# Kernel optimization log

Hardware: AMD Instinct MI355X
Metric: run time of the kernel (lower is better)

The kernel has to match this reference:

```python
import jax, jax.numpy as jnp
import numpy as np

NUM_GRAPHS = 64
NODE_SZ = 200
FEAT = 200
HID = 256          # hidden_size; each signed branch outputs HID//2
HALF = HID // 2
N_NODES = NUM_GRAPHS * NODE_SZ
N_EDGES = 409600
NUM_LAYERS = 3


def _lin_init(key, out_f, in_f):
    kw, kb = jax.random.split(key)
    s = 1.0 / np.sqrt(in_f)
    W = jax.random.uniform(kw, (out_f, in_f), minval=-s, maxval=s, dtype=jnp.float32)
    b = jax.random.uniform(kb, (out_f,), minval=-s, maxval=s, dtype=jnp.float32)
    return W, b


def setup_inputs() -> dict:
    key = jax.random.key(0)
    ks = jax.random.split(key, 16)
    x = jax.random.normal(ks[0], (N_NODES, FEAT), dtype=jnp.float32)
    edge_index = jax.random.randint(ks[1], (2, N_EDGES), 0, N_NODES, dtype=jnp.int64)
    edge_weight = jax.random.normal(ks[2], (N_EDGES,), dtype=jnp.float32)
    batch = jnp.repeat(jnp.arange(NUM_GRAPHS, dtype=jnp.int64), NODE_SZ)

    # signed conv layer params: layer0 in=FEAT, layers 1..: in=HID; each lin maps 2*in -> HALF
    Wp0, bp0 = _lin_init(ks[3], HALF, 2 * FEAT)
    Wn0, bn0 = _lin_init(ks[4], HALF, 2 * FEAT)
    Wp1, bp1 = _lin_init(ks[5], HALF, 2 * HID)
    Wn1, bn1 = _lin_init(ks[6], HALF, 2 * HID)
    Wp2, bp2 = _lin_init(ks[7], HALF, 2 * HID)
    Wn2, bn2 = _lin_init(ks[8], HALF, 2 * HID)
    Wr, br = _lin_init(ks[9], HID, NODE_SZ * HID)   # readout_lin
    Wl, bl = _lin_init(ks[10], 1, HID)              # final lin
    return dict(x=x, edge_index=edge_index, edge_weight=edge_weight, batch=batch,
                Wp0=Wp0, bp0=bp0, Wn0=Wn0, bn0=bn0,
                Wp1=Wp1, bp1=bp1, Wn1=Wn1, bn1=bn1,
                Wp2=Wp2, bp2=bp2, Wn2=Wn2, bn2=bn2,
                Wr=Wr, br=br, Wl=Wl, bl=bl)


def _signed_conv(x, src, dst, w, Wp, bp, Wn, bn):
    # edge-weighted signed mean aggregation, split by weight sign
    xs = x[src]                                   # [E, D] gather
    pw = jnp.where(w > 0, w, 0.0)
    nw = jnp.where(w < 0, -w, 0.0)
    agg_p = jax.ops.segment_sum(pw[:, None] * xs, dst, num_segments=N_NODES)
    agg_n = jax.ops.segment_sum(nw[:, None] * xs, dst, num_segments=N_NODES)
    deg_p = jax.ops.segment_sum((w > 0).astype(x.dtype), dst, num_segments=N_NODES)
    deg_n = jax.ops.segment_sum((w < 0).astype(x.dtype), dst, num_segments=N_NODES)
    agg_p = agg_p / jnp.maximum(deg_p, 1.0)[:, None]
    agg_n = agg_n / jnp.maximum(deg_n, 1.0)[:, None]
    hp = jnp.concatenate([agg_p, x], -1) @ Wp.T + bp
    hn = jnp.concatenate([agg_n, x], -1) @ Wn.T + bn
    return jnp.concatenate([hp, hn], -1)          # [N, HID]


def reference(x, edge_index, edge_weight, batch,
              Wp0, bp0, Wn0, bn0, Wp1, bp1, Wn1, bn1, Wp2, bp2, Wn2, bn2,
              Wr, br, Wl, bl):
    src, dst = edge_index[0], edge_index[1]
    convs = [(Wp0, bp0, Wn0, bn0), (Wp1, bp1, Wn1, bn1), (Wp2, bp2, Wn2, bn2)]
    h = x
    for i, (Wp, bp, Wn, bn) in enumerate(convs):
        h = _signed_conv(h, src, dst, edge_weight, Wp, bp, Wn, bn)
        if i < NUM_LAYERS - 1:
            h = jax.nn.leaky_relu(h, negative_slope=0.01)
    # per-graph readout: batch is contiguous with NODE_SZ nodes per graph,
    # so the boolean-mask+view loop is exactly a reshape.
    g = h.reshape(NUM_GRAPHS, NODE_SZ * HID)
    g = g @ Wr.T + br                             # [G, HID]
    # dropout(p=0.5) is identity in eval mode
    return g @ Wl.T + bl                          # [G, 1]
```

## Files before the change

kernel.cpp:

```cpp
#include <hip/hip_runtime.h>

#define NUM_GRAPHS 64
#define NODE_SZ    200
#define FEAT       200
#define HID        256
#define HALF       128
#define N_NODES    (NUM_GRAPHS * NODE_SZ)
#define KREAD      (NODE_SZ * HID)
#define HBLK       128

typedef unsigned short ushort_t;
typedef unsigned int uint_t;
typedef __attribute__((ext_vector_type(8))) short bf16x8;
typedef __attribute__((ext_vector_type(4))) float f32x4;

#define GAS(p) ((const __attribute__((address_space(1))) void*)(p))
#define LAS(p) ((__attribute__((address_space(3))) void*)(p))

__device__ __forceinline__ float bf2f(ushort_t u) {
    union { unsigned int i; float f; } v; v.i = ((unsigned int)u) << 16; return v.f;
}
__device__ __forceinline__ ushort_t f2bf(float f) {
    union { float f; unsigned int i; } v; v.f = f;
    unsigned int x = v.i;
    unsigned int r = (x + 0x7fffu + ((x >> 16) & 1u)) >> 16;
    return (ushort_t)r;
}

__global__ __launch_bounds__(1024) void bhist_kernel(const int* __restrict__ ei,
                                                     const float* __restrict__ ew,
                                                     uint_t* __restrict__ bh, int E) {
    __shared__ uint_t h[N_NODES];
    for (int i = threadIdx.x; i < N_NODES; i += 1024) h[i] = 0;
    __syncthreads();
    int b = blockIdx.x;
    int epb = (E + HBLK - 1) / HBLK;
    int e0 = b * epb, e1 = min(e0 + epb, E);
    for (int e = e0 + threadIdx.x; e < e1; e += 1024) {
        int dst = ei[E + e];
        float w = ew[e];
        if (w > 0.0f)      atomicAdd(&h[dst], 1u);
        else if (w < 0.0f) atomicAdd(&h[dst], 0x10000u);
    }
    __syncthreads();
    uint_t* out = bh + (size_t)b * N_NODES;
    for (int i = threadIdx.x * 4; i < N_NODES; i += 4096)
        *(uint4*)&out[i] = *(const uint4*)&h[i];
}

__global__ void colpref_kernel(uint_t* __restrict__ bh, int* __restrict__ counts,
                               int* __restrict__ cnt_p) {
    int n = blockIdx.x * 256 + threadIdx.x;
    if (n >= N_NODES) return;
    uint_t seq = 0;
#pragma unroll 1
    for (int b = 0; b < HBLK; b += 8) {
        uint_t v[8];
#pragma unroll
        for (int j = 0; j < 8; ++j) v[j] = bh[(size_t)(b + j) * N_NODES + n];
#pragma unroll
        for (int j = 0; j < 8; ++j) {
            bh[(size_t)(b + j) * N_NODES + n] = seq;
            seq += v[j];
        }
    }
    counts[n] = (int)((seq & 0xffffu) + (seq >> 16));
    cnt_p[n]  = (int)(seq & 0xffffu);
}

__global__ __launch_bounds__(1024) void scan_kernel(const int* __restrict__ counts,
                                                    const int* __restrict__ cnt_p,
                                                    uint2* __restrict__ obnd, int n) {
    const int PER = 13;
    int t = threadIdx.x;
    int start = t * PER;
    int local[PER];
    int sum = 0;
#pragma unroll
    for (int i = 0; i < PER; ++i) {
        int idx = start + i;
        int v = (idx < n) ? counts[idx] : 0;
        local[i] = sum;
        sum += v;
    }
    int lane = t & 63, wid = t >> 6;
    int inc = sum;
#pragma unroll
    for (int d = 1; d < 64; d <<= 1) {
        int up = __shfl_up(inc, d);
        if (lane >= d) inc += up;
    }
    __shared__ int wsum[16], woff[16];
    if (lane == 63) wsum[wid] = inc;
    __syncthreads();
    if (t < 16) {
        int acc = 0;
        for (int j = 0; j < 16; ++j) if (j < t) acc += wsum[j];
        woff[t] = acc;
    }
    __syncthreads();
    int base = woff[wid] + (inc - sum);
#pragma unroll
    for (int i = 0; i < PER; ++i) {
        int idx = start + i;
        if (idx < n) {
            uint_t off = (uint_t)(base + local[i]);
            obnd[idx] = make_uint2(off, off + (uint_t)cnt_p[idx]);
        }
    }
    if (t == 1023) {
        uint_t tot = (uint_t)(base + sum);
        obnd[n] = make_uint2(tot, tot);
    }
}

__global__ __launch_bounds__(1024) void scat_prep_kernel(
        const int* __restrict__ ei, const float* __restrict__ ew,
        const uint_t* __restrict__ bh, const uint2* __restrict__ obnd,
        uint2* __restrict__ es, int E,
        const float* __restrict__ W0p, const float* __restrict__ W0n,
        const float* __restrict__ W1p, const float* __restrict__ W1n,
        const float* __restrict__ W2p, const float* __restrict__ W2n,
        const float* __restrict__ x,
        ushort_t* __restrict__ wall, ushort_t* __restrict__ xb) {
    __shared__ uint_t cur[N_NODES];
    int bx = blockIdx.x;
    if (bx < HBLK) {
        const uint_t* pref = bh + (size_t)bx * N_NODES;
        for (int i = threadIdx.x * 4; i < N_NODES; i += 4096)
            *(uint4*)&cur[i] = *(const uint4*)&pref[i];
        __syncthreads();
        int epb = (E + HBLK - 1) / HBLK;
        int e0 = bx * epb, e1 = min(e0 + epb, E);
        for (int e = e0 + threadIdx.x; e < e1; e += 1024) {
            int src = ei[e];
            int dst = ei[E + e];
            float w = ew[e];
            if (w > 0.0f) {
                uint_t old = atomicAdd(&cur[dst], 1u);
                uint_t pos = obnd[dst].x + (old & 0xffffu);
                es[pos] = make_uint2((uint_t)src, __float_as_uint(w));
            } else if (w < 0.0f) {
                uint_t old = atomicAdd(&cur[dst], 0x10000u);
                uint_t pos = obnd[dst].y + (old >> 16);
                es[pos] = make_uint2((uint_t)src, __float_as_uint(-w));
            }
        }
    } else if (bx < 512) {
        int idx = (bx - 128) * 1024 + threadIdx.x;
        int layer = idx >> 17;
        int within = idx & 131071;
        int rr = within >> 8;
        int col = within & 255;
        const float* Wp = (layer == 0) ? W0p : (layer == 1) ? W1p : W2p;
        const float* Wn = (layer == 0) ? W0n : (layer == 1) ? W1n : W2n;
        int Ks = (layer == 0) ? 200 : 256;
        int q = rr >> 7;
        const float* Wsrc = (q & 1) ? Wn : Wp;
        int row = rr & 127;
        int scol = col + ((q >> 1) ? Ks : 0);
        float v = (col < Ks) ? Wsrc[(size_t)row * (2 * Ks) + scol] : 0.0f;
        wall[idx] = f2bf(v);
    } else {
        int idx = (bx - 512) * 1024 + threadIdx.x;
        int n = idx >> 6;
        int c0 = (idx & 63) * 4;
        ushort4 o = {0, 0, 0, 0};
        if (c0 < 200) {
            float4 v = *(const float4*)&x[(size_t)n * 200 + c0];
            o.x = f2bf(v.x); o.y = f2bf(v.y); o.z = f2bf(v.z); o.w = f2bf(v.w);
        }
        *(ushort4*)&xb[(size_t)n * 256 + c0] = o;
    }
}

template <int KSTEPS>
__global__ __launch_bounds__(256) void gemm_mfma(
        const ushort_t* __restrict__ A,
        const ushort_t* __restrict__ B,
        ushort_t* __restrict__ Y) {
    __shared__ __align__(16) ushort_t As[2][32 * 32];
    __shared__ __align__(16) ushort_t Bs[2][128 * 32];
    int mBase = blockIdx.x * 32;
    int nBase = blockIdx.y * 128;
    int tid  = threadIdx.x;
    int lane = tid & 63;
    int wv   = tid >> 6;
    int r    = lane & 15;
    int quad = lane >> 4;

    int rowA = tid >> 2, colA = (tid & 3) * 8;
    const ushort_t* gA  = A + (size_t)(mBase + (rowA & 31)) * 256 + colA;
    const ushort_t* gB0 = B + (size_t)(nBase + rowA) * 256 + colA;
    const ushort_t* gB1 = B + (size_t)(nBase + rowA + 64) * 256 + colA;

    f32x4 acc00 = {0.f,0.f,0.f,0.f}, acc01 = {0.f,0.f,0.f,0.f};
    f32x4 acc10 = {0.f,0.f,0.f,0.f}, acc11 = {0.f,0.f,0.f,0.f};

    if (tid < 128)
        __builtin_amdgcn_global_load_lds(GAS(gA), LAS(&As[0][wv * 512]), 16, 0, 0);
    __builtin_amdgcn_global_load_lds(GAS(gB0), LAS(&Bs[0][wv * 512]), 16, 0, 0);
    __builtin_amdgcn_global_load_lds(GAS(gB1), LAS(&Bs[0][2048 + wv * 512]), 16, 0, 0);

    for (int kt = 0; kt < KSTEPS; ++kt) {
        int cur = kt & 1;
        __syncthreads();
        if (kt + 1 < KSTEPS) {
            int kB = (kt + 1) * 32;
            if (tid < 128)
                __builtin_amdgcn_global_load_lds(GAS(gA + kB), LAS(&As[cur ^ 1][wv * 512]), 16, 0, 0);
            __builtin_amdgcn_global_load_lds(GAS(gB0 + kB), LAS(&Bs[cur ^ 1][wv * 512]), 16, 0, 0);
            __builtin_amdgcn_global_load_lds(GAS(gB1 + kB), LAS(&Bs[cur ^ 1][2048 + wv * 512]), 16, 0, 0);
        }
        bf16x8 a0 = *(const bf16x8*)&As[cur][r * 32 + quad * 8];
        bf16x8 a1 = *(const bf16x8*)&As[cur][(16 + r) * 32 + quad * 8];
        bf16x8 b0 = *(const bf16x8*)&Bs[cur][(wv * 32 + r) * 32 + quad * 8];
        bf16x8 b1 = *(const bf16x8*)&Bs[cur][(wv * 32 + 16 + r) * 32 + quad * 8];
        acc00 = __builtin_amdgcn_mfma_f32_16x16x32_bf16(a0, b0, acc00, 0, 0, 0);
        acc01 = __builtin_amdgcn_mfma_f32_16x16x32_bf16(a0, b1, acc01, 0, 0, 0);
        acc10 = __builtin_amdgcn_mfma_f32_16x16x32_bf16(a1, b0, acc10, 0, 0, 0);
        acc11 = __builtin_amdgcn_mfma_f32_16x16x32_bf16(a1, b1, acc11, 0, 0, 0);
    }
#pragma unroll
    for (int jn = 0; jn < 2; ++jn) {
        int cl = nBase + wv * 32 + jn * 16 + r;
        f32x4 am0 = jn ? acc01 : acc00;
        f32x4 am1 = jn ? acc11 : acc10;
#pragma unroll
        for (int reg = 0; reg < 4; ++reg) {
            int m0 = mBase + quad * 4 + reg;
            Y[(size_t)m0 * 512 + cl]        = f2bf(am0[reg]);
            Y[(size_t)(m0 + 16) * 512 + cl] = f2bf(am1[reg]);
        }
    }
}

template <bool LEAKY>
__global__ __launch_bounds__(256) void aggcomb_kernel(
        const ushort_t* __restrict__ Y,
        const uint2* __restrict__ obnd,
        const uint2* __restrict__ es,
        const float* __restrict__ bp, const float* __restrict__ bn,
        ushort_t* __restrict__ out) {
    int lane = threadIdx.x & 63;
    int wv   = threadIdx.x >> 6;
    int n = blockIdx.x * 4 + wv;
    int c0 = lane * 2;
    uint2 ob = obnd[n];
    uint_t off = ob.x, mid = ob.y, end = obnd[n + 1].x;

    float accp[2] = {0.f, 0.f};
    float accn[2] = {0.f, 0.f};

#pragma unroll 1
    for (int phase = 0; phase < 2; ++phase) {
        uint_t lo = phase ? mid : off;
        uint_t hi = phase ? end : mid;
        float* acc = phase ? accn : accp;
        const ushort_t* Yb = Y + (phase ? 128 : 0) + c0;
#pragma unroll 1
        for (uint_t base = lo; base < hi; base += 64) {
            int cnt = (int)min(64u, hi - base);
            uint2 rec = es[base + (uint_t)min(lane, cnt - 1)];
            int i = 0;
#pragma unroll 1
            for (; i + 8 <= cnt; i += 8) {
                int s[8]; float w[8]; uint_t u[8];
#pragma unroll
                for (int j = 0; j < 8; ++j) {
                    s[j] = __shfl((int)rec.x, i + j);
                    w[j] = __uint_as_float((uint_t)__shfl((int)rec.y, i + j));
                }
#pragma unroll
                for (int j = 0; j < 8; ++j) u[j] = *(const uint_t*)&Yb[(size_t)s[j] * 512];
#pragma unroll
                for (int j = 0; j < 8; ++j) {
                    acc[0] = fmaf(w[j], bf2f((ushort_t)(u[j] & 0xffffu)), acc[0]);
                    acc[1] = fmaf(w[j], bf2f((ushort_t)(u[j] >> 16)), acc[1]);
                }
            }
#pragma unroll 1
            for (; i < cnt; ++i) {
                int s = __shfl((int)rec.x, i);
                float w = __uint_as_float((uint_t)__shfl((int)rec.y, i));
                uint_t u = *(const uint_t*)&Yb[(size_t)s * 512];
                acc[0] = fmaf(w, bf2f((ushort_t)(u & 0xffffu)), acc[0]);
                acc[1] = fmaf(w, bf2f((ushort_t)(u >> 16)), acc[1]);
            }
        }
    }

    float dp = fmaxf((float)(mid - off), 1.0f);
    float dn = fmaxf((float)(end - mid), 1.0f);
    float rp = 1.0f / dp, rn = 1.0f / dn;
    uint_t zp = *(const uint_t*)&Y[(size_t)n * 512 + 256 + c0];
    uint_t zn = *(const uint_t*)&Y[(size_t)n * 512 + 384 + c0];
    float vp0 = fmaf(accp[0], rp, bf2f((ushort_t)(zp & 0xffffu)) + bp[c0]);
    float vp1 = fmaf(accp[1], rp, bf2f((ushort_t)(zp >> 16))     + bp[c0 + 1]);
    float vn0 = fmaf(accn[0], rn, bf2f((ushort_t)(zn & 0xffffu)) + bn[c0]);
    float vn1 = fmaf(accn[1], rn, bf2f((ushort_t)(zn >> 16))     + bn[c0 + 1]);
    if (LEAKY) {
        vp0 = (vp0 > 0.0f) ? vp0 : 0.01f * vp0;
        vp1 = (vp1 > 0.0f) ? vp1 : 0.01f * vp1;
        vn0 = (vn0 > 0.0f) ? vn0 : 0.01f * vn0;
        vn1 = (vn1 > 0.0f) ? vn1 : 0.01f * vn1;
    }
    uint_t op = (uint_t)f2bf(vp0) | ((uint_t)f2bf(vp1) << 16);
    uint_t on = (uint_t)f2bf(vn0) | ((uint_t)f2bf(vn1) << 16);
    *(uint_t*)&out[(size_t)n * 256 + c0]       = op;
    *(uint_t*)&out[(size_t)n * 256 + 128 + c0] = on;
}

__global__ __launch_bounds__(256) void readout_mfma(
        const ushort_t* __restrict__ h, const float* __restrict__ Wr,
        float* __restrict__ partial) {
    __shared__ __align__(16) ushort_t As[64 * 32];
    __shared__ __align__(16) ushort_t Bs[64 * 32];
    int nBase  = blockIdx.x * 64;
    int kStart = blockIdx.y * 800;
    int tid  = threadIdx.x;
    int lane = tid & 63;
    int wv   = tid >> 6;
    int r    = lane & 15;
    int quad = lane >> 4;

    f32x4 acc[4];
#pragma unroll
    for (int j = 0; j < 4; ++j) acc[j] = (f32x4){0.f, 0.f, 0.f, 0.f};

    for (int kt = 0; kt < 25; ++kt) {
        int kBase = kStart + kt * 32;
        int lin = tid * 8;
        int row = lin >> 5, col = lin & 31;
        *(uint4*)&As[lin] = *(const uint4*)&h[(size_t)row * KREAD + kBase + col];
        {
            const float* wp = &Wr[(size_t)(nBase + row) * KREAD + kBase + col];
            float4 f0 = *(const float4*)&wp[0];
            float4 f1 = *(const float4*)&wp[4];
            ushort4 b0, b1;
            b0.x = f2bf(f0.x); b0.y = f2bf(f0.y); b0.z = f2bf(f0.z); b0.w = f2bf(f0.w);
            b1.x = f2bf(f1.x); b1.y = f2bf(f1.y); b1.z = f2bf(f1.z); b1.w = f2bf(f1.w);
            *(ushort4*)&Bs[lin]     = b0;
            *(ushort4*)&Bs[lin + 4] = b1;
        }
        __syncthreads();
        bf16x8 a = *(const bf16x8*)&As[(wv * 16 + r) * 32 + quad * 8];
#pragma unroll
        for (int j = 0; j < 4; ++j) {
            bf16x8 b = *(const bf16x8*)&Bs[(j * 16 + r) * 32 + quad * 8];
            acc[j] = __builtin_amdgcn_mfma_f32_16x16x32_bf16(a, b, acc[j], 0, 0, 0);
        }
        __syncthreads();
    }
    float* out = partial + (size_t)blockIdx.y * (64 * HID);
#pragma unroll
    for (int j = 0; j < 4; ++j) {
        int c = nBase + j * 16 + r;
#pragma unroll
        for (int reg = 0; reg < 4; ++reg) {
            int g = wv * 16 + quad * 4 + reg;
            out[g * HID + c] = acc[j][reg];
        }
    }
}

__global__ void final_kernel(const float* __restrict__ partial, const float* __restrict__ br,
                             const float* __restrict__ Wl, const float* __restrict__ bl,
                             float* __restrict__ out) {
    int g = blockIdx.x;
    int c = threadIdx.x;
    float s = 0.0f;
#pragma unroll 4
    for (int k = 0; k < 64; ++k) s += partial[(size_t)k * (64 * HID) + g * HID + c];
    float v = (s + br[c]) * Wl[c];
#pragma unroll
    for (int d = 32; d > 0; d >>= 1) v += __shfl_down(v, d);
    __shared__ float sh[4];
    if ((c & 63) == 0) sh[c >> 6] = v;
    __syncthreads();
    if (c == 0) out[g] = sh[0] + sh[1] + sh[2] + sh[3] + bl[0];
}

extern "C" void kernel_launch(void* const* d_in, const int* in_sizes, int n_in,
                              void* d_out, int out_size, void* d_ws, size_t ws_size,
                              hipStream_t stream) {
    const float* x  = (const float*)d_in[0];
    const int*   ei = (const int*)d_in[1];
    const float* ew = (const float*)d_in[2];
    const float* Wp0 = (const float*)d_in[4];
    const float* bp0 = (const float*)d_in[5];
    const float* Wn0 = (const float*)d_in[6];
    const float* bn0 = (const float*)d_in[7];
    const float* Wp1 = (const float*)d_in[8];
    const float* bp1 = (const float*)d_in[9];
    const float* Wn1 = (const float*)d_in[10];
    const float* bn1 = (const float*)d_in[11];
    const float* Wp2 = (const float*)d_in[12];
    const float* bp2 = (const float*)d_in[13];
    const float* Wn2 = (const float*)d_in[14];
    const float* bn2 = (const float*)d_in[15];
    const float* Wr  = (const float*)d_in[16];
    const float* br  = (const float*)d_in[17];
    const float* Wl  = (const float*)d_in[18];
    const float* bl  = (const float*)d_in[19];
    const int E = in_sizes[1] / 2;

    char* ws = (char*)d_ws;
    float*    partial = (float*)(ws + 0);
    uint_t*   bh      = (uint_t*)(ws + 4194304);
    int*      counts  = (int*)(ws + 10747904);
    int*      cnt_p   = (int*)(ws + 10799104);
    uint2*    obnd    = (uint2*)(ws + 10850304);
    uint2*    es      = (uint2*)(ws + 10952768);
    ushort_t* Yall    = (ushort_t*)(ws + 14229568);
    ushort_t* hA      = (ushort_t*)(ws + 27336768);
    ushort_t* hB      = (ushort_t*)(ws + 33890368);
    ushort_t* wall    = (ushort_t*)(ws + 40443968);
    ushort_t* xb      = (ushort_t*)(ws + 41230400);

    hipLaunchKernelGGL(bhist_kernel, dim3(HBLK), dim3(1024), 0, stream, ei, ew, bh, E);
    hipLaunchKernelGGL(colpref_kernel, dim3((N_NODES + 255) / 256), dim3(256), 0, stream,
                       bh, counts, cnt_p);
    hipLaunchKernelGGL(scan_kernel, dim3(1), dim3(1024), 0, stream, counts, cnt_p, obnd, N_NODES);
    hipLaunchKernelGGL(scat_prep_kernel, dim3(1312), dim3(1024), 0, stream,
                       ei, ew, bh, obnd, es, E,
                       Wp0, Wn0, Wp1, Wn1, Wp2, Wn2, x, wall, xb);

    hipLaunchKernelGGL((gemm_mfma<7>), dim3(N_NODES / 32, 4), dim3(256), 0, stream,
                       xb, wall + 0 * 131072, Yall);
    hipLaunchKernelGGL((aggcomb_kernel<true>), dim3(N_NODES / 4), dim3(256), 0, stream,
                       Yall, obnd, es, bp0, bn0, hA);
    hipLaunchKernelGGL((gemm_mfma<8>), dim3(N_NODES / 32, 4), dim3(256), 0, stream,
                       hA, wall + 1 * 131072, Yall);
    hipLaunchKernelGGL((aggcomb_kernel<true>), dim3(N_NODES / 4), dim3(256), 0, stream,
                       Yall, obnd, es, bp1, bn1, hB);
    hipLaunchKernelGGL((gemm_mfma<8>), dim3(N_NODES / 32, 4), dim3(256), 0, stream,
                       hB, wall + 2 * 131072, Yall);
    hipLaunchKernelGGL((aggcomb_kernel<false>), dim3(N_NODES / 4), dim3(256), 0, stream,
                       Yall, obnd, es, bp2, bn2, hA);

    hipLaunchKernelGGL(readout_mfma, dim3(4, 64), dim3(256), 0, stream, hA, Wr, partial);
    hipLaunchKernelGGL(final_kernel, dim3(NUM_GRAPHS), dim3(256), 0, stream,
                       partial, br, Wl, bl, (float*)d_out);
}
```

Baseline: 296.8 us.

## Fuse whole pipeline into one persistent kernel with software grid barriers

Replaces the chain of about a dozen kernel launches with an init kernel plus one persistent mega-kernel of 256 blocks. Phases are separated by flag-based global barriers. The CSR build now uses global atomics for the histogram and a two-level block scan instead of per-block LDS histograms. The GEMM is retiled to 128x256 tiles over 200 tiles, and aggregation uses a grid-stride loop. This removes launch gaps and per-kernel tail effects. In exchange it risks barrier spin cost and global atomic contention, and it relies on all 256 blocks being co-resident, which a barrier with a timeout cap does not guarantee.

Result: slower. 1.176 ms (+296.3%).

```diff
diff --git a/kernel.cpp b/kernel.cpp
--- a/kernel.cpp
+++ b/kernel.cpp
@@ -7,7 +7,8 @@
 #define HALF       128
 #define N_NODES    (NUM_GRAPHS * NODE_SZ)
 #define KREAD      (NODE_SZ * HID)
-#define HBLK       128
+#define NBLK       256
+#define NTHR       512
 
 typedef unsigned short ushort_t;
 typedef unsigned int uint_t;
@@ -27,313 +28,190 @@
     return (ushort_t)r;
 }
 
-__global__ __launch_bounds__(1024) void bhist_kernel(const int* __restrict__ ei,
-                                                     const float* __restrict__ ew,
-                                                     uint_t* __restrict__ bh, int E) {
-    __shared__ uint_t h[N_NODES];
-    for (int i = threadIdx.x; i < N_NODES; i += 1024) h[i] = 0;
+__device__ __forceinline__ void gbar(uint_t* __restrict__ flags, int k) {
+    __threadfence();
     __syncthreads();
-    int b = blockIdx.x;
-    int epb = (E + HBLK - 1) / HBLK;
-    int e0 = b * epb, e1 = min(e0 + epb, E);
-    for (int e = e0 + threadIdx.x; e < e1; e += 1024) {
-        int dst = ei[E + e];
-        float w = ew[e];
-        if (w > 0.0f)      atomicAdd(&h[dst], 1u);
-        else if (w < 0.0f) atomicAdd(&h[dst], 0x10000u);
+    if (threadIdx.x == 0)
+        __hip_atomic_store(&flags[(k << 8) | blockIdx.x], 1u,
+                           __ATOMIC_RELAXED, __HIP_MEMORY_SCOPE_AGENT);
+    if (threadIdx.x < NBLK) {
+        int cap = 0;
+        while (__hip_atomic_load(&flags[(k << 8) | threadIdx.x],
+                                 __ATOMIC_RELAXED, __HIP_MEMORY_SCOPE_AGENT) == 0u) {
+            __builtin_amdgcn_s_sleep(2);
+            if (++cap > (1 << 18)) break;
+        }
     }
     __syncthreads();
-    uint_t* out = bh + (size_t)b * N_NODES;
-    for (int i = threadIdx.x * 4; i < N_NODES; i += 4096)
-        *(uint4*)&out[i] = *(const uint4*)&h[i];
-}
-
-__global__ void colpref_kernel(uint_t* __restrict__ bh, int* __restrict__ counts,
-                               int* __restrict__ cnt_p) {
-    int n = blockIdx.x * 256 + threadIdx.x;
-    if (n >= N_NODES) return;
-    uint_t seq = 0;
-#pragma unroll 1
-    for (int b = 0; b < HBLK; b += 8) {
-        uint_t v[8];
-#pragma unroll
-        for (int j = 0; j < 8; ++j) v[j] = bh[(size_t)(b + j) * N_NODES + n];
-#pragma unroll
-        for (int j = 0; j < 8; ++j) {
-            bh[(size_t)(b + j) * N_NODES + n] = seq;
-            seq += v[j];
-        }
-    }
-    counts[n] = (int)((seq & 0xffffu) + (seq >> 16));
-    cnt_p[n]  = (int)(seq & 0xffffu);
-}
-
-__global__ __launch_bounds__(1024) void scan_kernel(const int* __restrict__ counts,
-                                                    const int* __restrict__ cnt_p,
-                                                    uint2* __restrict__ obnd, int n) {
-    const int PER = 13;
-    int t = threadIdx.x;
-    int start = t * PER;
-    int local[PER];
-    int sum = 0;
-#pragma unroll
-    for (int i = 0; i < PER; ++i) {
-        int idx = start + i;
-        int v = (idx < n) ? counts[idx] : 0;
-        local[i] = sum;
-        sum += v;
-    }
-    int lane = t & 63, wid = t >> 6;
-    int inc = sum;
-#pragma unroll
-    for (int d = 1; d < 64; d <<= 1) {
-        int up = __shfl_up(inc, d);
-        if (lane >= d) inc += up;
-    }
-    __shared__ int wsum[16], woff[16];
-    if (lane == 63) wsum[wid] = inc;
-    __syncthreads();
-    if (t < 16) {
-        int acc = 0;
-        for (int j = 0; j < 16; ++j) if (j < t) acc += wsum[j];
-        woff[t] = acc;
-    }
-    __syncthreads();
-    int base = woff[wid] + (inc - sum);
-#pragma unroll
-    for (int i = 0; i < PER; ++i) {
-        int idx = start + i;
-        if (idx < n) {
-            uint_t off = (uint_t)(base + local[i]);
-            obnd[idx] = make_uint2(off, off + (uint_t)cnt_p[idx]);
-        }
-    }
-    if (t == 1023) {
-        uint_t tot = (uint_t)(base + sum);
-        obnd[n] = make_uint2(tot, tot);
-    }
-}
-
-__global__ __launch_bounds__(1024) void scat_prep_kernel(
-        const int* __restrict__ ei, const float* __restrict__ ew,
-        const uint_t* __restrict__ bh, const uint2* __restrict__ obnd,
-        uint2* __restrict__ es, int E,
-        const float* __restrict__ W0p, const float* __restrict__ W0n,
-        const float* __restrict__ W1p, const float* __restrict__ W1n,
-        const float* __restrict__ W2p, const float* __restrict__ W2n,
-        const float* __restrict__ x,
-        ushort_t* __restrict__ wall, ushort_t* __restrict__ xb) {
-    __shared__ uint_t cur[N_NODES];
-    int bx = blockIdx.x;
-    if (bx < HBLK) {
-        const uint_t* pref = bh + (size_t)bx * N_NODES;
-        for (int i = threadIdx.x * 4; i < N_NODES; i += 4096)
-            *(uint4*)&cur[i] = *(const uint4*)&pref[i];
-        __syncthreads();
-        int epb = (E + HBLK - 1) / HBLK;
-        int e0 = bx * epb, e1 = min(e0 + epb, E);
-        for (int e = e0 + threadIdx.x; e < e1; e += 1024) {
-            int src = ei[e];
-            int dst = ei[E + e];
-            float w = ew[e];
-            if (w > 0.0f) {
-                uint_t old = atomicAdd(&cur[dst], 1u);
-                uint_t pos = obnd[dst].x + (old & 0xffffu);
-                es[pos] = make_uint2((uint_t)src, __float_as_uint(w));
-            } else if (w < 0.0f) {
-                uint_t old = atomicAdd(&cur[dst], 0x10000u);
-                uint_t pos = obnd[dst].y + (old >> 16);
-                es[pos] = make_uint2((uint_t)src, __float_as_uint(-w));
-            }
-        }
-    } else if (bx < 512) {
-        int idx = (bx - 128) * 1024 + threadIdx.x;
-        int layer = idx >> 17;
-        int within = idx & 131071;
-        int rr = within >> 8;
-        int col = within & 255;
-        const float* Wp = (layer == 0) ? W0p : (layer == 1) ? W1p : W2p;
-        const float* Wn = (layer == 0) ? W0n : (layer == 1) ? W1n : W2n;
-        int Ks = (layer == 0) ? 200 : 256;
-        int q = rr >> 7;
-        const float* Wsrc = (q & 1) ? Wn : Wp;
-        int row = rr & 127;
-        int scol = col + ((q >> 1) ? Ks : 0);
-        float v = (col < Ks) ? Wsrc[(size_t)row * (2 * Ks) + scol] : 0.0f;
-        wall[idx] = f2bf(v);
-    } else {
-        int idx = (bx - 512) * 1024 + threadIdx.x;
-        int n = idx >> 6;
-        int c0 = (idx & 63) * 4;
-        ushort4 o = {0, 0, 0, 0};
-        if (c0 < 200) {
-            float4 v = *(const float4*)&x[(size_t)n * 200 + c0];
-            o.x = f2bf(v.x); o.y = f2bf(v.y); o.z = f2bf(v.z); o.w = f2bf(v.w);
-        }
-        *(ushort4*)&xb[(size_t)n * 256 + c0] = o;
-    }
-}
-
-template <int KSTEPS>
-__global__ __launch_bounds__(256) void gemm_mfma(
-        const ushort_t* __restrict__ A,
-        const ushort_t* __restrict__ B,
-        ushort_t* __restrict__ Y) {
-    __shared__ __align__(16) ushort_t As[2][32 * 32];
-    __shared__ __align__(16) ushort_t Bs[2][128 * 32];
-    int mBase = blockIdx.x * 32;
-    int nBase = blockIdx.y * 128;
+    __threadfence();
+}
+
+__device__ __forceinline__ void gemm_phase(const ushort_t* __restrict__ A,
+                                           const ushort_t* __restrict__ Bw,
+                                           ushort_t* __restrict__ Y,
+                                           ushort_t* smem) {
+    int t = blockIdx.x;
+    if (t >= 200) return;
+    int mBase = (t >> 1) * 128;
+    int nBase = (t & 1) * 256;
     int tid  = threadIdx.x;
     int lane = tid & 63;
     int wv   = tid >> 6;
     int r    = lane & 15;
     int quad = lane >> 4;
-
-    int rowA = tid >> 2, colA = (tid & 3) * 8;
-    const ushort_t* gA  = A + (size_t)(mBase + (rowA & 31)) * 256 + colA;
-    const ushort_t* gB0 = B + (size_t)(nBase + rowA) * 256 + colA;
-    const ushort_t* gB1 = B + (size_t)(nBase + rowA + 64) * 256 + colA;
-
-    f32x4 acc00 = {0.f,0.f,0.f,0.f}, acc01 = {0.f,0.f,0.f,0.f};
-    f32x4 acc10 = {0.f,0.f,0.f,0.f}, acc11 = {0.f,0.f,0.f,0.f};
-
-    if (tid < 128)
-        __builtin_amdgcn_global_load_lds(GAS(gA), LAS(&As[0][wv * 512]), 16, 0, 0);
-    __builtin_amdgcn_global_load_lds(GAS(gB0), LAS(&Bs[0][wv * 512]), 16, 0, 0);
-    __builtin_amdgcn_global_load_lds(GAS(gB1), LAS(&Bs[0][2048 + wv * 512]), 16, 0, 0);
-
-    for (int kt = 0; kt < KSTEPS; ++kt) {
-        int cur = kt & 1;
+    int wm   = wv >> 1;
+    int wn   = wv & 1;
+
+    int rowA = tid >> 2, colc = (tid & 3) * 8;
+    const ushort_t* gA  = A  + (size_t)(mBase + rowA) * 256 + colc;
+    const ushort_t* gB0 = Bw + (size_t)(nBase + rowA) * 256 + colc;
+    const ushort_t* gB1 = Bw + (size_t)(nBase + 128 + rowA) * 256 + colc;
+
+    f32x4 acc[2][8];
+#pragma unroll
+    for (int i = 0; i < 2; ++i)
+#pragma unroll
+        for (int j = 0; j < 8; ++j) acc[i][j] = (f32x4){0.f, 0.f, 0.f, 0.f};
+
+    auto STAGE = [&](int buf, int kb) {
+        ushort_t* Ad = smem + (buf << 12) + tid * 8;
+        ushort_t* Bd = smem + 8192 + (buf << 13) + tid * 8;
+        __builtin_amdgcn_global_load_lds(GAS(gA + kb), LAS(Ad), 16, 0, 0);
+        __builtin_amdgcn_global_load_lds(GAS(gB0 + kb), LAS(Bd), 16, 0, 0);
+        __builtin_amdgcn_global_load_lds(GAS(gB1 + kb), LAS(Bd + 4096), 16, 0, 0);
+    };
+
+    STAGE(0, 0);
+    for (int kt = 0; kt < 8; ++kt) {
+        int cb = kt & 1;
         __syncthreads();
-        if (kt + 1 < KSTEPS) {
-            int kB = (kt + 1) * 32;
-            if (tid < 128)
-                __builtin_amdgcn_global_load_lds(GAS(gA + kB), LAS(&As[cur ^ 1][wv * 512]), 16, 0, 0);
-            __builtin_amdgcn_global_load_lds(GAS(gB0 + kB), LAS(&Bs[cur ^ 1][wv * 512]), 16, 0, 0);
-            __builtin_amdgcn_global_load_lds(GAS(gB1 + kB), LAS(&Bs[cur ^ 1][2048 + wv * 512]), 16, 0, 0);
-        }
-        bf16x8 a0 = *(const bf16x8*)&As[cur][r * 32 + quad * 8];
-        bf16x8 a1 = *(const bf16x8*)&As[cur][(16 + r) * 32 + quad * 8];
-        bf16x8 b0 = *(const bf16x8*)&Bs[cur][(wv * 32 + r) * 32 + quad * 8];
-        bf16x8 b1 = *(const bf16x8*)&Bs[cur][(wv * 32 + 16 + r) * 32 + quad * 8];
-        acc00 = __builtin_amdgcn_mfma_f32_16x16x32_bf16(a0, b0, acc00, 0, 0, 0);
-        acc01 = __builtin_amdgcn_mfma_f32_16x16x32_bf16(a0, b1, acc01, 0, 0, 0);
-        acc10 = __builtin_amdgcn_mfma_f32_16x16x32_bf16(a1, b0, acc10, 0, 0, 0);
-        acc11 = __builtin_amdgcn_mfma_f32_16x16x32_bf16(a1, b1, acc11, 0, 0, 0);
-    }
-#pragma unroll
-    for (int jn = 0; jn < 2; ++jn) {
-        int cl = nBase + wv * 32 + jn * 16 + r;
-        f32x4 am0 = jn ? acc01 : acc00;
-        f32x4 am1 = jn ? acc11 : acc10;
-#pragma unroll
-        for (int reg = 0; reg < 4; ++reg) {
-            int m0 = mBase + quad * 4 + reg;
-            Y[(size_t)m0 * 512 + cl]        = f2bf(am0[reg]);
-            Y[(size_t)(m0 + 16) * 512 + cl] = f2bf(am1[reg]);
-        }
-    }
-}
-
-template <bool LEAKY>
-__global__ __launch_bounds__(256) void aggcomb_kernel(
-        const ushort_t* __restrict__ Y,
-        const uint2* __restrict__ obnd,
-        const uint2* __restrict__ es,
-        const float* __restrict__ bp, const float* __restrict__ bn,
-        ushort_t* __restrict__ out) {
+        if (kt < 7) STAGE(cb ^ 1, (kt + 1) * 32);
+        const ushort_t* Ac = smem + (cb << 12);
+        const ushort_t* Bc = smem + 8192 + (cb << 13);
+        bf16x8 af[2];
+#pragma unroll
+        for (int i = 0; i < 2; ++i)
+            af[i] = *(const bf16x8*)&Ac[(wm * 32 + i * 16 + r) * 32 + quad * 8];
+#pragma unroll
+        for (int j = 0; j < 8; ++j) {
+            bf16x8 bfr = *(const bf16x8*)&Bc[(wn * 128 + j * 16 + r) * 32 + quad * 8];
+            acc[0][j] = __builtin_amdgcn_mfma_f32_16x16x32_bf16(af[0], bfr, acc[0][j], 0, 0, 0);
+            acc[1][j] = __builtin_amdgcn_mfma_f32_16x16x32_bf16(af[1], bfr, acc[1][j], 0, 0, 0);
+        }
+    }
+#pragma unroll
+    for (int i = 0; i < 2; ++i)
+#pragma unroll
+        for (int j = 0; j < 8; ++j) {
+            int c = nBase + wn * 128 + j * 16 + r;
+#pragma unroll
+            for (int reg = 0; reg < 4; ++reg) {
+                int m = mBase + wm * 32 + i * 16 + quad * 4 + reg;
+                Y[(size_t)m * 512 + c] = f2bf(acc[i][j][reg]);
+            }
+        }
+}
+
+__device__ __forceinline__ void agg_phase(const ushort_t* __restrict__ Y,
+                                          const uint2* __restrict__ obnd,
+                                          const uint2* __restrict__ es,
+                                          const float* __restrict__ bp,
+                                          const float* __restrict__ bn,
+                                          ushort_t* __restrict__ outp, bool leaky) {
     int lane = threadIdx.x & 63;
-    int wv   = threadIdx.x >> 6;
-    int n = blockIdx.x * 4 + wv;
     int c0 = lane * 2;
-    uint2 ob = obnd[n];
-    uint_t off = ob.x, mid = ob.y, end = obnd[n + 1].x;
-
-    float accp[2] = {0.f, 0.f};
-    float accn[2] = {0.f, 0.f};
-
+    int nw = gridDim.x << 3;
+    for (int n = (blockIdx.x << 3) + (threadIdx.x >> 6); n < N_NODES; n += nw) {
+        uint2 ob = obnd[n];
+        uint_t off = ob.x, mid = ob.y, end = obnd[n + 1].x;
+        float accp[2] = {0.f, 0.f};
+        float accn[2] = {0.f, 0.f};
 #pragma unroll 1
-    for (int phase = 0; phase < 2; ++phase) {
-        uint_t lo = phase ? mid : off;
-        uint_t hi = phase ? end : mid;
-        float* acc = phase ? accn : accp;
-        const ushort_t* Yb = Y + (phase ? 128 : 0) + c0;
+        for (int phase = 0; phase < 2; ++phase) {
+            uint_t lo = phase ? mid : off;
+            uint_t hi = phase ? end : mid;
+            float* acc = phase ? accn : accp;
+            const ushort_t* Yb = Y + (phase ? 128 : 0) + c0;
 #pragma unroll 1
-        for (uint_t base = lo; base < hi; base += 64) {
-            int cnt = (int)min(64u, hi - base);
-            uint2 rec = es[base + (uint_t)min(lane, cnt - 1)];
-            int i = 0;
+            for (uint_t base = lo; base < hi; base += 64) {
+                int cnt = (int)min(64u, hi - base);
+                uint2 rec = es[base + (uint_t)min(lane, cnt - 1)];
+                int i = 0;
 #pragma unroll 1
-            for (; i + 8 <= cnt; i += 8) {
-                int s[8]; float w[8]; uint_t u[8];
-#pragma unroll
-                for (int j = 0; j < 8; ++j) {
-                    s[j] = __shfl((int)rec.x, i + j);
-                    w[j] = __uint_as_float((uint_t)__shfl((int)rec.y, i + j));
+                for (; i + 8 <= cnt; i += 8) {
+                    int s[8]; float w[8]; uint_t u[8];
+#pragma unroll
+                    for (int j = 0; j < 8; ++j) {
+                        s[j] = __shfl((int)rec.x, i + j);
+                        w[j] = __uint_as_float((uint_t)__shfl((int)rec.y, i + j));
+                    }
+#pragma unroll
+                    for (int j = 0; j < 8; ++j) u[j] = *(const uint_t*)&Yb[(size_t)s[j] * 512];
+#pragma unroll
+                    for (int j = 0; j < 8; ++j) {
+                        acc[0] = fmaf(w[j], bf2f((ushort_t)(u[j] & 0xffffu)), acc[0]);
+                        acc[1] = fmaf(w[j], bf2f((ushort_t)(u[j] >> 16)), acc[1]);
+                    }
                 }
-#pragma unroll
-                for (int j = 0; j < 8; ++j) u[j] = *(const uint_t*)&Yb[(size_t)s[j] * 512];
-#pragma unroll
-                for (int j = 0; j < 8; ++j) {
-                    acc[0] = fmaf(w[j], bf2f((ushort_t)(u[j] & 0xffffu)), acc[0]);
-                    acc[1] = fmaf(w[j], bf2f((ushort_t)(u[j] >> 16)), acc[1]);
+#pragma unroll 1
+                for (; i < cnt; ++i) {
+                    int s = __shfl((int)rec.x, i);
+                    float w = __uint_as_float((uint_t)__shfl((int)rec.y, i));
+                    uint_t u = *(const uint_t*)&Yb[(size_t)s * 512];
+                    acc[0] = fmaf(w, bf2f((ushort_t)(u & 0xffffu)), acc[0]);
+                    acc[1] = fmaf(w, bf2f((ushort_t)(u >> 16)), acc[1]);
                 }
             }
-#pragma unroll 1
-            for (; i < cnt; ++i) {
-                int s = __shfl((int)rec.x, i);
-                float w = __uint_as_float((uint_t)__shfl((int)rec.y, i));
-                uint_t u = *(const uint_t*)&Yb[(size_t)s * 512];
-                acc[0] = fmaf(w, bf2f((ushort_t)(u & 0xffffu)), acc[0]);
-                acc[1] = fmaf(w, bf2f((ushort_t)(u >> 16)), acc[1]);
-            }
-        }
-    }
-
-    float dp = fmaxf((float)(mid - off), 1.0f);
-    float dn = fmaxf((float)(end - mid), 1.0f);
-    float rp = 1.0f / dp, rn = 1.0f / dn;
-    uint_t zp = *(const uint_t*)&Y[(size_t)n * 512 + 256 + c0];
-    uint_t zn = *(const uint_t*)&Y[(size_t)n * 512 + 384 + c0];
-    float vp0 = fmaf(accp[0], rp, bf2f((ushort_t)(zp & 0xffffu)) + bp[c0]);
-    float vp1 = fmaf(accp[1], rp, bf2f((ushort_t)(zp >> 16))     + bp[c0 + 1]);
-    float vn0 = fmaf(accn[0], rn, bf2f((ushort_t)(zn & 0xffffu)) + bn[c0]);
-    float vn1 = fmaf(accn[1], rn, bf2f((ushort_t)(zn >> 16))     + bn[c0 + 1]);
-    if (LEAKY) {
-        vp0 = (vp0 > 0.0f) ? vp0 : 0.01f * vp0;
-        vp1 = (vp1 > 0.0f) ? vp1 : 0.01f * vp1;
-        vn0 = (vn0 > 0.0f) ? vn0 : 0.01f * vn0;
-        vn1 = (vn1 > 0.0f) ? vn1 : 0.01f * vn1;
-    }
-    uint_t op = (uint_t)f2bf(vp0) | ((uint_t)f2bf(vp1) << 16);
-    uint_t on = (uint_t)f2bf(vn0) | ((uint_t)f2bf(vn1) << 16);
-    *(uint_t*)&out[(size_t)n * 256 + c0]       = op;
-    *(uint_t*)&out[(size_t)n * 256 + 128 + c0] = on;
-}
-
-__global__ __launch_bounds__(256) void readout_mfma(
-        const ushort_t* __restrict__ h, const float* __restrict__ Wr,
-        float* __restrict__ partial) {
-    __shared__ __align__(16) ushort_t As[64 * 32];
-    __shared__ __align__(16) ushort_t Bs[64 * 32];
-    int nBase  = blockIdx.x * 64;
-    int kStart = blockIdx.y * 800;
+        }
+        float dp = fmaxf((float)(mid - off), 1.0f);
+        float dn = fmaxf((float)(end - mid), 1.0f);
+        float rp = 1.0f / dp, rn = 1.0f / dn;
+        uint_t zp = *(const uint_t*)&Y[(size_t)n * 512 + 256 + c0];
+        uint_t zn = *(const uint_t*)&Y[(size_t)n * 512 + 384 + c0];
+        float vp0 = fmaf(accp[0], rp, bf2f((ushort_t)(zp & 0xffffu)) + bp[c0]);
+        float vp1 = fmaf(accp[1], rp, bf2f((ushort_t)(zp >> 16))     + bp[c0 + 1]);
+        float vn0 = fmaf(accn[0], rn, bf2f((ushort_t)(zn & 0xffffu)) + bn[c0]);
+        float vn1 = fmaf(accn[1], rn, bf2f((ushort_t)(zn >> 16))     + bn[c0 + 1]);
+        if (leaky) {
+            vp0 = (vp0 > 0.0f) ? vp0 : 0.01f * vp0;
+            vp1 = (vp1 > 0.0f) ? vp1 : 0.01f * vp1;
+            vn0 = (vn0 > 0.0f) ? vn0 : 0.01f * vn0;
+            vn1 = (vn1 > 0.0f) ? vn1 : 0.01f * vn1;
+        }
+        uint_t op = (uint_t)f2bf(vp0) | ((uint_t)f2bf(vp1) << 16);
+        uint_t on = (uint_t)f2bf(vn0) | ((uint_t)f2bf(vn1) << 16);
+        *(uint_t*)&outp[(size_t)n * 256 + c0]       = op;
+        *(uint_t*)&outp[(size_t)n * 256 + 128 + c0] = on;
+    }
+}
+
+__device__ __forceinline__ void readout_phase(const ushort_t* __restrict__ h,
+                                              const float* __restrict__ Wr,
+                                              float* __restrict__ partial,
+                                              ushort_t* smem) {
+    ushort_t* As = smem;
+    ushort_t* Bs = smem + 2048;
+    int b = blockIdx.x;
+    int nBase  = (b & 3) * 64;
+    int kStart = (b >> 2) * 800;
     int tid  = threadIdx.x;
     int lane = tid & 63;
     int wv   = tid >> 6;
     int r    = lane & 15;
     int quad = lane >> 4;
-
-    f32x4 acc[4];
-#pragma unroll
-    for (int j = 0; j < 4; ++j) acc[j] = (f32x4){0.f, 0.f, 0.f, 0.f};
+    int wm   = wv >> 1;
+    int wn   = wv & 1;
+
+    f32x4 acc[2];
+    acc[0] = (f32x4){0.f, 0.f, 0.f, 0.f};
+    acc[1] = (f32x4){0.f, 0.f, 0.f, 0.f};
 
     for (int kt = 0; kt < 25; ++kt) {
         int kBase = kStart + kt * 32;
-        int lin = tid * 8;
-        int row = lin >> 5, col = lin & 31;
-        *(uint4*)&As[lin] = *(const uint4*)&h[(size_t)row * KREAD + kBase + col];
-        {
+        if (tid < 256) {
+            int lin = tid * 8;
+            int row = lin >> 5, col = lin & 31;
+            *(uint4*)&As[lin] = *(const uint4*)&h[(size_t)row * KREAD + kBase + col];
             const float* wp = &Wr[(size_t)(nBase + row) * KREAD + kBase + col];
             float4 f0 = *(const float4*)&wp[0];
             float4 f1 = *(const float4*)&wp[4];
@@ -344,41 +222,188 @@
             *(ushort4*)&Bs[lin + 4] = b1;
         }
         __syncthreads();
-        bf16x8 a = *(const bf16x8*)&As[(wv * 16 + r) * 32 + quad * 8];
-#pragma unroll
-        for (int j = 0; j < 4; ++j) {
-            bf16x8 b = *(const bf16x8*)&Bs[(j * 16 + r) * 32 + quad * 8];
-            acc[j] = __builtin_amdgcn_mfma_f32_16x16x32_bf16(a, b, acc[j], 0, 0, 0);
+        bf16x8 a = *(const bf16x8*)&As[(wm * 16 + r) * 32 + quad * 8];
+#pragma unroll
+        for (int j = 0; j < 2; ++j) {
+            bf16x8 bb = *(const bf16x8*)&Bs[(wn * 32 + j * 16 + r) * 32 + quad * 8];
+            acc[j] = __builtin_amdgcn_mfma_f32_16x16x32_bf16(a, bb, acc[j], 0, 0, 0);
         }
         __syncthreads();
     }
-    float* out = partial + (size_t)blockIdx.y * (64 * HID);
-#pragma unroll
-    for (int j = 0; j < 4; ++j) {
-        int c = nBase + j * 16 + r;
+    float* o = partial + (size_t)(b >> 2) * (64 * HID);
+#pragma unroll
+    for (int j = 0; j < 2; ++j) {
+        int c = nBase + wn * 32 + j * 16 + r;
 #pragma unroll
         for (int reg = 0; reg < 4; ++reg) {
-            int g = wv * 16 + quad * 4 + reg;
-            out[g * HID + c] = acc[j][reg];
-        }
-    }
-}
-
-__global__ void final_kernel(const float* __restrict__ partial, const float* __restrict__ br,
-                             const float* __restrict__ Wl, const float* __restrict__ bl,
-                             float* __restrict__ out) {
+            int g = wm * 16 + quad * 4 + reg;
+            o[g * HID + c] = acc[j][reg];
+        }
+    }
+}
+
+__device__ __forceinline__ void final_phase(const float* __restrict__ partial,
+                                            const float* __restrict__ br,
+                                            const float* __restrict__ Wl,
+                                            const float* __restrict__ bl,
+                                            float* __restrict__ out, float* shf) {
     int g = blockIdx.x;
-    int c = threadIdx.x;
-    float s = 0.0f;
+    if (g >= NUM_GRAPHS) return;
+    int tid = threadIdx.x;
+    if (tid < 256) {
+        int c = tid;
+        float s = 0.0f;
 #pragma unroll 4
-    for (int k = 0; k < 64; ++k) s += partial[(size_t)k * (64 * HID) + g * HID + c];
-    float v = (s + br[c]) * Wl[c];
-#pragma unroll
-    for (int d = 32; d > 0; d >>= 1) v += __shfl_down(v, d);
-    __shared__ float sh[4];
-    if ((c & 63) == 0) sh[c >> 6] = v;
+        for (int k = 0; k < 64; ++k) s += partial[(size_t)k * (64 * HID) + g * HID + c];
+        float v = (s + br[c]) * Wl[c];
+#pragma unroll
+        for (int d = 32; d > 0; d >>= 1) v += __shfl_down(v, d);
+        if ((c & 63) == 0) shf[c >> 6] = v;
+    }
     __syncthreads();
-    if (c == 0) out[g] = sh[0] + sh[1] + sh[2] + sh[3] + bl[0];
+    if (tid == 0) out[g] = shf[0] + shf[1] + shf[2] + shf[3] + bl[0];
+}
+
+__global__ __launch_bounds__(512) void init_kernel(uint_t* __restrict__ flags,
+                                                   uint_t* __restrict__ cnt,
+                                                   uint_t* __restrict__ cur) {
+    int i = blockIdx.x * 512 + threadIdx.x;
+    int GS = gridDim.x * 512;
+    for (int k = i; k < 16 * NBLK; k += GS) flags[k] = 0u;
+    for (int k = i; k < N_NODES; k += GS) { cnt[k] = 0u; cur[k] = 0u; }
+}
+
+__global__ __launch_bounds__(NTHR, 2) void mega_kernel(
+        const float* __restrict__ x, const int* __restrict__ ei, const float* __restrict__ ew,
+        const float* __restrict__ Wp0, const float* __restrict__ Wn0,
+        const float* __restrict__ Wp1, const float* __restrict__ Wn1,
+        const float* __restrict__ Wp2, const float* __restrict__ Wn2,
+        const float* __restrict__ bp0, const float* __restrict__ bn0,
+        const float* __restrict__ bp1, const float* __restrict__ bn1,
+        const float* __restrict__ bp2, const float* __restrict__ bn2,
+        const float* __restrict__ Wr, const float* __restrict__ br,
+        const float* __restrict__ Wl, const float* __restrict__ bl,
+        float* __restrict__ out, char* __restrict__ ws, int E) {
+    float*    partial = (float*)(ws);
+    uint_t*   cnt     = (uint_t*)(ws + 4194304);
+    uint_t*   cur     = (uint_t*)(ws + 4245504);
+    uint_t*   pref    = (uint_t*)(ws + 4296704);
+    uint_t*   bsum    = (uint_t*)(ws + 4347904);
+    uint2*    obnd    = (uint2*)(ws + 4349952);
+    uint2*    es      = (uint2*)(ws + 4452416);
+    ushort_t* Yall    = (ushort_t*)(ws + 7729216);
+    ushort_t* hA      = (ushort_t*)(ws + 20836416);
+    ushort_t* hB      = (ushort_t*)(ws + 27390016);
+    ushort_t* wall    = (ushort_t*)(ws + 33943616);
+    ushort_t* xb      = (ushort_t*)(ws + 34730048);
+    uint_t*   flags   = (uint_t*)(ws + 41283648);
+
+    __shared__ __align__(16) ushort_t smem[24576];
+
+    int tid = threadIdx.x;
+    int gid = blockIdx.x * NTHR + tid;
+    const int GSZ = NBLK * NTHR;
+
+    for (int idx = gid; idx < 3 * 131072; idx += GSZ) {
+        int layer = idx >> 17, within = idx & 131071;
+        int rr = within >> 8, col = within & 255;
+        const float* Wp = (layer == 0) ? Wp0 : (layer == 1) ? Wp1 : Wp2;
+        const float* Wn = (layer == 0) ? Wn0 : (layer == 1) ? Wn1 : Wn2;
+        int Ks = (layer == 0) ? 200 : 256;
+        int q = rr >> 7;
+        const float* Wsrc = (q & 1) ? Wn : Wp;
+        int row = rr & 127;
+        int scol = col + ((q >> 1) ? Ks : 0);
+        float v = (col < Ks) ? Wsrc[(size_t)row * (2 * Ks) + scol] : 0.0f;
+        wall[idx] = f2bf(v);
+    }
+    for (int idx = gid; idx < N_NODES * 64; idx += GSZ) {
+        int n = idx >> 6, c0 = (idx & 63) * 4;
+        ushort4 o = {0, 0, 0, 0};
+        if (c0 < 200) {
+            float4 v = *(const float4*)&x[(size_t)n * 200 + c0];
+            o.x = f2bf(v.x); o.y = f2bf(v.y); o.z = f2bf(v.z); o.w = f2bf(v.w);
+        }
+        *(ushort4*)&xb[(size_t)n * 256 + c0] = o;
+    }
+    for (int e = gid; e < E; e += GSZ) {
+        int dst = ei[E + e];
+        float w = ew[e];
+        if (w > 0.0f)      atomicAdd(&cnt[dst], 1u);
+        else if (w < 0.0f) atomicAdd(&cnt[dst], 0x10000u);
+    }
+    gbar(flags, 0);
+
+    if (tid < 64) {
+        int b = blockIdx.x, lane = tid;
+        int n = b * 50 + lane;
+        uint_t c = (lane < 50) ? cnt[n] : 0u;
+        uint_t tot = (c & 0xffffu) + (c >> 16);
+        uint_t inc = tot;
+#pragma unroll
+        for (int d = 1; d < 64; d <<= 1) {
+            uint_t up = (uint_t)__shfl_up((int)inc, d);
+            if (lane >= d) inc += up;
+        }
+        if (lane < 50) pref[n] = inc - tot;
+        if (lane == 63) bsum[b] = inc;
+    }
+    gbar(flags, 1);
+
+    if (tid < 64) {
+        int b = blockIdx.x, lane = tid;
+        uint_t sB = 0, sA = 0;
+#pragma unroll
+        for (int j0 = 0; j0 < 256; j0 += 64) {
+            uint_t v = bsum[j0 + lane];
+            sA += v;
+            if (j0 + lane < b) sB += v;
+        }
+#pragma unroll
+        for (int d = 32; d > 0; d >>= 1) {
+            sB += (uint_t)__shfl_xor((int)sB, d);
+            sA += (uint_t)__shfl_xor((int)sA, d);
+        }
+        if (lane < 50) {
+            int n = b * 50 + lane;
+            uint_t off = sB + pref[n];
+            uint_t pc = cnt[n] & 0xffffu;
+            obnd[n] = make_uint2(off, off + pc);
+        }
+        if (b == 0 && lane == 0) obnd[N_NODES] = make_uint2(sA, sA);
+    }
+    gbar(flags, 2);
+
+    for (int e = gid; e < E; e += GSZ) {
+        int src = ei[e];
+        int dst = ei[E + e];
+        float w = ew[e];
+        if (w > 0.0f) {
+            uint_t old = atomicAdd(&cur[dst], 1u);
+            es[obnd[dst].x + (old & 0xffffu)] = make_uint2((uint_t)src, __float_as_uint(w));
+        } else if (w < 0.0f) {
+            uint_t old = atomicAdd(&cur[dst], 0x10000u);
+            es[obnd[dst].y + (old >> 16)] = make_uint2((uint_t)src, __float_as_uint(-w));
+        }
+    }
+    gemm_phase(xb, wall, Yall, smem);
+    gbar(flags, 3);
+
+    agg_phase(Yall, obnd, es, bp0, bn0, hA, true);
+    gbar(flags, 4);
+    gemm_phase(hA, wall + 131072, Yall, smem);
+    gbar(flags, 5);
+    agg_phase(Yall, obnd, es, bp1, bn1, hB, true);
+    gbar(flags, 6);
+    gemm_phase(hB, wall + 262144, Yall, smem);
+    gbar(flags, 7);
+    agg_phase(Yall, obnd, es, bp2, bn2, hA, false);
+    gbar(flags, 8);
+
+    readout_phase(hA, Wr, partial, smem);
+    gbar(flags, 9);
+
+    final_phase(partial, br, Wl, bl, out, (float*)smem);
 }
 
 extern "C" void kernel_launch(void* const* d_in, const int* in_sizes, int n_in,
@@ -403,43 +428,18 @@
     const float* br  = (const float*)d_in[17];
     const float* Wl  = (const float*)d_in[18];
     const float* bl  = (const float*)d_in[19];
-    const int E = in_sizes[1] / 2;
+    int E = in_sizes[1] / 2;
 
     char* ws = (char*)d_ws;
-    float*    partial = (float*)(ws + 0);
-    uint_t*   bh      = (uint_t*)(ws + 4194304);
-    int*      counts  = (int*)(ws + 10747904);
-    int*      cnt_p   = (int*)(ws + 10799104);
-    uint2*    obnd    = (uint2*)(ws + 10850304);
-    uint2*    es      = (uint2*)(ws + 10952768);
-    ushort_t* Yall    = (ushort_t*)(ws + 14229568);
-    ushort_t* hA      = (ushort_t*)(ws + 27336768);
-    ushort_t* hB      = (ushort_t*)(ws + 33890368);
-    ushort_t* wall    = (ushort_t*)(ws + 40443968);
-    ushort_t* xb      = (ushort_t*)(ws + 41230400);
-
-    hipLaunchKernelGGL(bhist_kernel, dim3(HBLK), dim3(1024), 0, stream, ei, ew, bh, E);
-    hipLaunchKernelGGL(colpref_kernel, dim3((N_NODES + 255) / 256), dim3(256), 0, stream,
-                       bh, counts, cnt_p);
-    hipLaunchKernelGGL(scan_kernel, dim3(1), dim3(1024), 0, stream, counts, cnt_p, obnd, N_NODES);
-    hipLaunchKernelGGL(scat_prep_kernel, dim3(1312), dim3(1024), 0, stream,
-                       ei, ew, bh, obnd, es, E,
-                       Wp0, Wn0, Wp1, Wn1, Wp2, Wn2, x, wall, xb);
-
-    hipLaunchKernelGGL((gemm_mfma<7>), dim3(N_NODES / 32, 4), dim3(256), 0, stream,
-                       xb, wall + 0 * 131072, Yall);
-    hipLaunchKernelGGL((aggcomb_kernel<true>), dim3(N_NODES / 4), dim3(256), 0, stream,
-                       Yall, obnd, es, bp0, bn0, hA);
-    hipLaunchKernelGGL((gemm_mfma<8>), dim3(N_NODES / 32, 4), dim3(256), 0, stream,
-                       hA, wall + 1 * 131072, Yall);
-    hipLaunchKernelGGL((aggcomb_kernel<true>), dim3(N_NODES / 4), dim3(256), 0, stream,
-                       Yall, obnd, es, bp1, bn1, hB);
-    hipLaunchKernelGGL((gemm_mfma<8>), dim3(N_NODES / 32, 4), dim3(256), 0, stream,
-                       hB, wall + 2 * 131072, Yall);
-    hipLaunchKernelGGL((aggcomb_kernel<false>), dim3(N_NODES / 4), dim3(256), 0, stream,
-                       Yall, obnd, es, bp2, bn2, hA);
-
-    hipLaunchKernelGGL(readout_mfma, dim3(4, 64), dim3(256), 0, stream, hA, Wr, partial);
-    hipLaunchKernelGGL(final_kernel, dim3(NUM_GRAPHS), dim3(256), 0, stream,
-                       partial, br, Wl, bl, (float*)d_out);
-}
+    uint_t* flags = (uint_t*)(ws + 41283648);
+    uint_t* cnt   = (uint_t*)(ws + 4194304);
+    uint_t* cur   = (uint_t*)(ws + 4245504);
+
+    hipLaunchKernelGGL(init_kernel, dim3(64), dim3(512), 0, stream, flags, cnt, cur);
+    hipLaunchKernelGGL(mega_kernel, dim3(NBLK), dim3(NTHR), 0, stream,
+                       x, ei, ew,
+                       Wp0, Wn0, Wp1, Wn1, Wp2, Wn2,
+                       bp0, bn0, bp1, bn1, bp2, bn2,
+                       Wr, br, Wl, bl,
+                       (float*)d_out, ws, E);
+}
```
